# Kernel optimization log

Measured on AMD Instinct MI355X. Metric: run time of the kernel, lower is better.

Reference implementation:

```python
import jax, jax.numpy as jnp
import numpy as np

N = 20000      # atoms
E = 320000     # pairs (avg degree 16)
F = 64         # per-atom features
NRBF = 32      # radial basis functions
RC = 1.0       # maximum_interaction_radius


def _decompose(t):
    # X = I + A + S (irreducible decomposition of 3x3 tensors)
    diag_mean = jnp.diagonal(t, axis1=-2, axis2=-1).mean(-1)
    I = diag_mean[..., None, None] * jnp.eye(3, dtype=t.dtype)
    A = 0.5 * (t - jnp.swapaxes(t, -1, -2))
    S = 0.5 * (t + jnp.swapaxes(t, -1, -2)) - I
    return I, A, S


def _tnorm(t):
    # Frobenius norm^2 over the trailing 3x3 -> [N, F]
    return (t ** 2).sum((-2, -1))


def _lin_t(t, W):
    # channel-mixing linear on the feature axis of [N, F, 3, 3]
    return jnp.einsum('nfij,gf->ngij', t, W)


def setup_inputs():
    key = jax.random.key(0)
    ks = jax.random.split(key, 14)
    inp = {
        'X': jax.random.normal(ks[0], (N, F, 3, 3), jnp.float32) * 0.1,
        'pair_indices': jax.random.randint(ks[1], (2, E), 0, N, jnp.int32),
        'd_ij': jax.random.uniform(ks[2], (E, 1), jnp.float32),
        'radial_feature_vector': jax.random.normal(ks[3], (E, NRBF), jnp.float32),
        'atomic_charges': jax.random.normal(ks[4], (N,), jnp.float32) * 0.1,
        # mlp_scalar: NRBF -> F -> 2F -> 3F (Dense = Linear + activation)
        'W0': jax.random.normal(ks[5], (F, NRBF), jnp.float32) / np.sqrt(NRBF),
        'b0': jnp.zeros((F,), jnp.float32),
        'W1': jax.random.normal(ks[6], (2 * F, F), jnp.float32) / np.sqrt(F),
        'b1': jnp.zeros((2 * F,), jnp.float32),
        'W2': jax.random.normal(ks[7], (3 * F, 2 * F), jnp.float32) / np.sqrt(2 * F),
        'b2': jnp.zeros((3 * F,), jnp.float32),
        # 6 bias-free FxF tensor linears
        'Wt': jax.random.normal(ks[8], (6, F, F), jnp.float32) / np.sqrt(F),
    }
    return inp


def reference(X, pair_indices, d_ij, radial_feature_vector, atomic_charges,
              W0, b0, W1, b1, W2, b2, Wt):
    silu = jax.nn.silu
    n_atoms = X.shape[0]
    src = pair_indices[1]  # gathered
    dst = pair_indices[0]  # scattered (index_add_)

    # cosine cutoff, [E, 1]
    C = (0.5 * (jnp.cos(jnp.pi * d_ij / RC) + 1.0)
         * (d_ij < RC).astype(X.dtype)).reshape(-1, 1)

    h = silu(radial_feature_vector @ W0.T + b0)
    h = silu(h @ W1.T + b1)
    h = silu(h @ W2.T + b2)                 # [E, 3F]
    rfv = (h * C).reshape(-1, F, 3)          # [E, F, 3]

    X = X / (_tnorm(X) + 1.0)[..., None, None]
    I, A, S = _decompose(X)
    I = _lin_t(I, Wt[0])
    A = _lin_t(A, Wt[1])
    S = _lin_t(S, Wt[2])
    Y = I + A + S

    def mp(r, T):
        # gather-mul-scatter: [E,F,3,3] messages reduced to [N,F,3,3]
        msg = r[:, :, None, None] * T[src]
        return jax.ops.segment_sum(msg, dst, num_segments=n_atoms)

    msg = mp(rfv[..., 0], I) + mp(rfv[..., 1], A) + mp(rfv[..., 2], S)

    # O(3) group
    q = (1.0 + 0.1 * atomic_charges)[:, None, None, None]
    I, A, S = _decompose(q * (jnp.matmul(msg, Y) + jnp.matmul(Y, msg)))

    normp1 = (_tnorm(I + A + S) + 1.0)[..., None, None]
    I, A, S = I / normp1, A / normp1, S / normp1
    I = _lin_t(I, Wt[3])
    A = _lin_t(A, Wt[4])
    S = _lin_t(S, Wt[5])
    dX = I + A + S

    X = X + dX + q * jnp.matmul(dX, dX)
    return X
```

## Files before the change

### kernel.cpp

```cpp
#include <hip/hip_runtime.h>
#include <hip/hip_bf16.h>
#include <cmath>

#define N_ATOMS 20000
#define NE      320000
#define FDIM    64
#define NRBF    32
#define PI_F    3.14159265358979323846f

typedef __attribute__((ext_vector_type(8))) short bf16x8;
typedef __attribute__((ext_vector_type(4))) float f32x4;

#define MFMA16(a, b, c) __builtin_amdgcn_mfma_f32_16x16x32_bf16(a, b, c, 0, 0, 0)

__device__ __forceinline__ float silu(float x) {
    return x / (1.0f + __expf(-x));
}

__device__ __forceinline__ unsigned short f2bf_rne(float x) {
    unsigned u = __float_as_uint(x);
    u += 0x7fffu + ((u >> 16) & 1u);
    return (unsigned short)(u >> 16);
}

__device__ __forceinline__ void split8(const float* v, bf16x8& hi, bf16x8& lo) {
#pragma unroll
    for (int j = 0; j < 8; j++) {
        unsigned u = __float_as_uint(v[j]);
        float hf = __uint_as_float(u & 0xffff0000u);
        hi[j] = (short)(u >> 16);
        lo[j] = (short)f2bf_rne(v[j] - hf);
    }
}

__global__ void transpose_kernel(const float* __restrict__ Wt, float* __restrict__ wtT) {
    int idx = blockIdx.x * 256 + threadIdx.x;
    if (idx >= 24576) return;
    int k = idx >> 12;
    int r = idx & 4095;
    int g = r >> 6;
    int f = r & 63;
    wtT[k * 4096 + f * 64 + g] = Wt[idx];
}

__global__ void wfrag_kernel(const float* __restrict__ W0, const float* __restrict__ W1,
                             const float* __restrict__ W2,
                             unsigned short* __restrict__ f0h, unsigned short* __restrict__ f0l,
                             unsigned short* __restrict__ f1h, unsigned short* __restrict__ f1l,
                             unsigned short* __restrict__ f2h, unsigned short* __restrict__ f2l) {
    int idx = blockIdx.x * 256 + threadIdx.x;
    const float* W;
    unsigned short *fh, *fl;
    int t, K, NT;
    if (idx < 2048)       { W = W0; fh = f0h; fl = f0l; t = idx;         K = 32;  NT = 4; }
    else if (idx < 10240) { W = W1; fh = f1h; fl = f1l; t = idx - 2048;  K = 64;  NT = 8; }
    else if (idx < 34816) { W = W2; fh = f2h; fl = f2l; t = idx - 10240; K = 128; NT = 12; }
    else return;
    int j = t & 7;
    int lane = (t >> 3) & 63;
    int rest = t >> 9;
    int nt = rest % NT;
    int ks = rest / NT;
    int k = ks * 32 + ((lane >> 4) & 3) * 8 + j;
    int n = nt * 16 + (lane & 15);
    float w = W[n * K + k];
    unsigned u = __float_as_uint(w);
    float hf = __uint_as_float(u & 0xffff0000u);
    fh[t] = (unsigned short)(u >> 16);
    fl[t] = f2bf_rne(w - hf);
}

__global__ void hist_kernel(const int* __restrict__ dst, int* __restrict__ deg) {
    int e = blockIdx.x * 256 + threadIdx.x;
    if (e >= NE) return;
    atomicAdd(&deg[dst[e]], 1);
}

__global__ void scan_kernel(const int* __restrict__ deg, int* __restrict__ off) {
    __shared__ int part[1024];
    int t = threadIdx.x;
    const int CH = (N_ATOMS + 1023) / 1024;
    int base = t * CH;
    int s = 0;
    for (int i = 0; i < CH; i++) {
        int idx = base + i;
        if (idx < N_ATOMS) s += deg[idx];
    }
    part[t] = s;
    __syncthreads();
    for (int ofs = 1; ofs < 1024; ofs <<= 1) {
        int v = (t >= ofs) ? part[t - ofs] : 0;
        __syncthreads();
        part[t] += v;
        __syncthreads();
    }
    int run = (t == 0) ? 0 : part[t - 1];
    for (int i = 0; i < CH; i++) {
        int idx = base + i;
        if (idx < N_ATOMS) {
            off[idx] = run;
            run += deg[idx];
        }
    }
    if (t == 1023) off[N_ATOMS] = run;
}

__global__ void fill_kernel(const int* __restrict__ dst, const int* __restrict__ srcArr,
                            const int* __restrict__ off, int* __restrict__ cursor,
                            int* __restrict__ sbkt, int* __restrict__ slotOf) {
    int e = blockIdx.x * 256 + threadIdx.x;
    if (e >= NE) return;
    int d = dst[e];
    int pos = atomicAdd(&cursor[d], 1);
    int slot = off[d] + pos;
    sbkt[slot] = srcArr[e];
    slotOf[e] = slot;
}

#define H1S 68
#define H2S 132
__global__ __launch_bounds__(128) void mlp_mfma_kernel(
    const float* __restrict__ rfv, const float* __restrict__ dij,
    const float* __restrict__ b0, const float* __restrict__ b1, const float* __restrict__ b2,
    const unsigned short* __restrict__ f0h, const unsigned short* __restrict__ f0l,
    const unsigned short* __restrict__ f1h, const unsigned short* __restrict__ f1l,
    const unsigned short* __restrict__ f2h, const unsigned short* __restrict__ f2l,
    const int* __restrict__ slotOf,
    __hip_bfloat16* __restrict__ r) {
    __shared__ float h1s[2][32][H1S];
    __shared__ float h2s[2][32][H2S];
    const int w = threadIdx.x >> 6;
    const int lane = threadIdx.x & 63;
    const int q = lane >> 4;
    const int c = lane & 15;
    const int e0 = (blockIdx.x * 2 + w) * 32;
    float (*h1)[H1S] = h1s[w];
    float (*h2)[H2S] = h2s[w];

    {
        bf16x8 ah[2], al[2];
#pragma unroll
        for (int mt = 0; mt < 2; mt++) {
            float v[8];
            const float* p = rfv + (size_t)(e0 + mt * 16 + c) * 32 + q * 8;
            *(float4*)(v)     = *(const float4*)(p);
            *(float4*)(v + 4) = *(const float4*)(p + 4);
            split8(v, ah[mt], al[mt]);
        }
#pragma unroll
        for (int nt = 0; nt < 4; nt++) {
            float bias = b0[nt * 16 + c];
            f32x4 acc[2];
            acc[0] = {bias, bias, bias, bias};
            acc[1] = acc[0];
            bf16x8 bh = *(const bf16x8*)(f0h + (size_t)(nt * 64 + lane) * 8);
            bf16x8 bl = *(const bf16x8*)(f0l + (size_t)(nt * 64 + lane) * 8);
#pragma unroll
            for (int mt = 0; mt < 2; mt++) {
                acc[mt] = MFMA16(al[mt], bh, acc[mt]);
                acc[mt] = MFMA16(ah[mt], bl, acc[mt]);
                acc[mt] = MFMA16(ah[mt], bh, acc[mt]);
            }
#pragma unroll
            for (int mt = 0; mt < 2; mt++)
#pragma unroll
                for (int reg = 0; reg < 4; reg++)
                    h1[mt * 16 + q * 4 + reg][nt * 16 + c] = silu(acc[mt][reg]);
        }
    }

    {
        bf16x8 ah[2][2], al[2][2];
#pragma unroll
        for (int mt = 0; mt < 2; mt++)
#pragma unroll
            for (int ks = 0; ks < 2; ks++) {
                float v[8];
                const float* p = &h1[mt * 16 + c][ks * 32 + q * 8];
                *(float4*)(v)     = *(const float4*)(p);
                *(float4*)(v + 4) = *(const float4*)(p + 4);
                split8(v, ah[mt][ks], al[mt][ks]);
            }
#pragma unroll
        for (int nt = 0; nt < 8; nt++) {
            float bias = b1[nt * 16 + c];
            f32x4 acc[2];
            acc[0] = {bias, bias, bias, bias};
            acc[1] = acc[0];
#pragma unroll
            for (int ks = 0; ks < 2; ks++) {
                bf16x8 bh = *(const bf16x8*)(f1h + (size_t)((ks * 8 + nt) * 64 + lane) * 8);
                bf16x8 bl = *(const bf16x8*)(f1l + (size_t)((ks * 8 + nt) * 64 + lane) * 8);
#pragma unroll
                for (int mt = 0; mt < 2; mt++) {
                    acc[mt] = MFMA16(al[mt][ks], bh, acc[mt]);
                    acc[mt] = MFMA16(ah[mt][ks], bl, acc[mt]);
                    acc[mt] = MFMA16(ah[mt][ks], bh, acc[mt]);
                }
            }
#pragma unroll
            for (int mt = 0; mt < 2; mt++)
#pragma unroll
                for (int reg = 0; reg < 4; reg++)
                    h2[mt * 16 + q * 4 + reg][nt * 16 + c] = silu(acc[mt][reg]);
        }
    }

    {
        bf16x8 ah[2][4], al[2][4];
#pragma unroll
        for (int mt = 0; mt < 2; mt++)
#pragma unroll
            for (int ks = 0; ks < 4; ks++) {
                float v[8];
                const float* p = &h2[mt * 16 + c][ks * 32 + q * 8];
                *(float4*)(v)     = *(const float4*)(p);
                *(float4*)(v + 4) = *(const float4*)(p + 4);
                split8(v, ah[mt][ks], al[mt][ks]);
            }
        float cut[2][4];
        int srow[2][4];
#pragma unroll
        for (int mt = 0; mt < 2; mt++)
#pragma unroll
            for (int reg = 0; reg < 4; reg++) {
                int e = e0 + mt * 16 + q * 4 + reg;
                float d = dij[e];
                cut[mt][reg] = (d < 1.0f) ? 0.5f * (__cosf(PI_F * d) + 1.0f) : 0.0f;
                srow[mt][reg] = slotOf[e];
            }
#pragma unroll
        for (int nt = 0; nt < 12; nt++) {
            float bias = b2[nt * 16 + c];
            f32x4 acc[2];
            acc[0] = {bias, bias, bias, bias};
            acc[1] = acc[0];
#pragma unroll
            for (int ks = 0; ks < 4; ks++) {
                bf16x8 bh = *(const bf16x8*)(f2h + (size_t)((ks * 12 + nt) * 64 + lane) * 8);
                bf16x8 bl = *(const bf16x8*)(f2l + (size_t)((ks * 12 + nt) * 64 + lane) * 8);
#pragma unroll
                for (int mt = 0; mt < 2; mt++) {
                    acc[mt] = MFMA16(al[mt][ks], bh, acc[mt]);
                    acc[mt] = MFMA16(ah[mt][ks], bl, acc[mt]);
                    acc[mt] = MFMA16(ah[mt][ks], bh, acc[mt]);
                }
            }
#pragma unroll
            for (int mt = 0; mt < 2; mt++)
#pragma unroll
                for (int reg = 0; reg < 4; reg++)
                    r[(size_t)srow[mt][reg] * 192 + nt * 16 + c] =
                        __float2bfloat16(silu(acc[mt][reg]) * cut[mt][reg]);
        }
    }
}

__global__ __launch_bounds__(256) void lin1_kernel(
    const float* __restrict__ X, const float* __restrict__ wtT,
    float* __restrict__ comp, float* __restrict__ Yb) {
    __shared__ float lds[4][64 * 11];
    int w = threadIdx.x >> 6;
    int l = threadIdx.x & 63;
    int a = blockIdx.x * 4 + w;

    {
        const float* x = X + ((size_t)a * 64 + l) * 9;
        float v[9];
#pragma unroll
        for (int i = 0; i < 9; i++) v[i] = x[i];
        float t2 = 0.f;
#pragma unroll
        for (int i = 0; i < 9; i++) t2 += v[i] * v[i];
        float inv = 1.0f / (t2 + 1.0f);
#pragma unroll
        for (int i = 0; i < 9; i++) v[i] *= inv;
        float iso = (v[0] + v[4] + v[8]) * (1.0f / 3.0f);
        float* o = &lds[w][l * 11];
        o[0] = iso;
        o[1] = 0.5f * (v[1] - v[3]);
        o[2] = 0.5f * (v[2] - v[6]);
        o[3] = 0.5f * (v[5] - v[7]);
        o[4] = v[0] - iso;
        o[5] = 0.5f * (v[1] + v[3]);
        o[6] = 0.5f * (v[2] + v[6]);
        o[7] = v[4] - iso;
        o[8] = 0.5f * (v[5] + v[7]);
        o[9] = v[8] - iso;
    }
    __syncthreads();
    {
        int g = l;
        const float* w0 = wtT;
        const float* w1 = wtT + 4096;
        const float* w2 = wtT + 8192;
        float acc[10];
#pragma unroll
        for (int c = 0; c < 10; c++) acc[c] = 0.f;
        for (int f = 0; f < 64; f++) {
            float wI = w0[f * 64 + g];
            float wA = w1[f * 64 + g];
            float wS = w2[f * 64 + g];
            const float* rf = &lds[w][f * 11];
            acc[0] += wI * rf[0];
            acc[1] += wA * rf[1];
            acc[2] += wA * rf[2];
            acc[3] += wA * rf[3];
#pragma unroll
            for (int c = 4; c < 10; c++) acc[c] += wS * rf[c];
        }
        float* co = comp + ((size_t)a * 64 + g) * 12;
        float4 c0 = {acc[0], acc[1], acc[2], acc[3]};
        float4 c1 = {acc[4], acc[5], acc[6], acc[7]};
        float4 c2 = {acc[8], acc[9], 0.f, 0.f};
        *(float4*)(co)     = c0;
        *(float4*)(co + 4) = c1;
        *(float4*)(co + 8) = c2;
        float* y = Yb + ((size_t)a * 64 + g) * 9;
        y[0] = acc[0] + acc[4];
        y[1] = acc[5] + acc[1];
        y[2] = acc[6] + acc[2];
        y[3] = acc[5] - acc[1];
        y[4] = acc[0] + acc[7];
        y[5] = acc[8] + acc[3];
        y[6] = acc[6] - acc[2];
        y[7] = acc[8] - acc[3];
        y[8] = acc[0] + acc[9];
    }
}

__global__ __launch_bounds__(256) void msg_lin2_kernel(
    const int* __restrict__ off, const int* __restrict__ sbkt,
    const __hip_bfloat16* __restrict__ r,
    const float* __restrict__ comp, const float* __restrict__ Yb,
    const float* __restrict__ X, const float* __restrict__ charges,
    const float* __restrict__ wtT, float* __restrict__ out) {
    __shared__ float lds[4][64 * 11];
    int w = threadIdx.x >> 6;
    int l = threadIdx.x & 63;
    int a = blockIdx.x * 4 + w;
    float q = 1.0f + 0.1f * charges[a];

    float m[10];
#pragma unroll
    for (int c = 0; c < 10; c++) m[c] = 0.f;
    {
        int beg = off[a], end = off[a + 1];
        if (beg < end) {
            __hip_bfloat16 ra, rb, rc;
            float4 c0, c1, c2;
            {
                const __hip_bfloat16* rp = r + (size_t)beg * 192 + l * 3;
                ra = rp[0]; rb = rp[1]; rc = rp[2];
                const float* cp = comp + ((size_t)sbkt[beg] * 64 + l) * 12;
                c0 = *(const float4*)(cp);
                c1 = *(const float4*)(cp + 4);
                c2 = *(const float4*)(cp + 8);
            }
            for (int i = beg + 1; i < end; i++) {
                const __hip_bfloat16* rp = r + (size_t)i * 192 + l * 3;
                __hip_bfloat16 na = rp[0], nb = rp[1], nc = rp[2];
                const float* cp = comp + ((size_t)sbkt[i] * 64 + l) * 12;
                float4 n0 = *(const float4*)(cp);
                float4 n1 = *(const float4*)(cp + 4);
                float4 n2 = *(const float4*)(cp + 8);
                float r0 = __bfloat162float(ra);
                float r1 = __bfloat162float(rb);
                float r2 = __bfloat162float(rc);
                m[0] += r0 * c0.x;
                m[1] += r1 * c0.y;
                m[2] += r1 * c0.z;
                m[3] += r1 * c0.w;
                m[4] += r2 * c1.x;
                m[5] += r2 * c1.y;
                m[6] += r2 * c1.z;
                m[7] += r2 * c1.w;
                m[8] += r2 * c2.x;
                m[9] += r2 * c2.y;
                ra = na; rb = nb; rc = nc;
                c0 = n0; c1 = n1; c2 = n2;
            }
            float r0 = __bfloat162float(ra);
            float r1 = __bfloat162float(rb);
            float r2 = __bfloat162float(rc);
            m[0] += r0 * c0.x;
            m[1] += r1 * c0.y;
            m[2] += r1 * c0.z;
            m[3] += r1 * c0.w;
            m[4] += r2 * c1.x;
            m[5] += r2 * c1.y;
            m[6] += r2 * c1.z;
            m[7] += r2 * c1.w;
            m[8] += r2 * c2.x;
            m[9] += r2 * c2.y;
        }
    }

    {
        float M[9];
        M[0] = m[0] + m[4]; M[1] = m[5] + m[1]; M[2] = m[6] + m[2];
        M[3] = m[5] - m[1]; M[4] = m[0] + m[7]; M[5] = m[8] + m[3];
        M[6] = m[6] - m[2]; M[7] = m[8] - m[3]; M[8] = m[0] + m[9];
        const float* yp = Yb + ((size_t)a * 64 + l) * 9;
        float Y[9];
#pragma unroll
        for (int i = 0; i < 9; i++) Y[i] = yp[i];
        float P[9];
#pragma unroll
        for (int i = 0; i < 3; i++) {
#pragma unroll
            for (int j = 0; j < 3; j++) {
                float s = 0.f;
#pragma unroll
                for (int k = 0; k < 3; k++)
                    s += M[i * 3 + k] * Y[k * 3 + j] + Y[i * 3 + k] * M[k * 3 + j];
                P[i * 3 + j] = q * s;
            }
        }
        float t2 = 0.f;
#pragma unroll
        for (int i = 0; i < 9; i++) t2 += P[i] * P[i];
        float inv = 1.0f / (t2 + 1.0f);
        float iso = (P[0] + P[4] + P[8]) * (1.0f / 3.0f);
        float* o = &lds[w][l * 11];
        o[0] = iso * inv;
        o[1] = 0.5f * (P[1] - P[3]) * inv;
        o[2] = 0.5f * (P[2] - P[6]) * inv;
        o[3] = 0.5f * (P[5] - P[7]) * inv;
        o[4] = (P[0] - iso) * inv;
        o[5] = 0.5f * (P[1] + P[3]) * inv;
        o[6] = 0.5f * (P[2] + P[6]) * inv;
        o[7] = (P[4] - iso) * inv;
        o[8] = 0.5f * (P[5] + P[7]) * inv;
        o[9] = (P[8] - iso) * inv;
    }
    __syncthreads();
    {
        int g = l;
        const float* w3 = wtT + 3 * 4096;
        const float* w4 = wtT + 4 * 4096;
        const float* w5 = wtT + 5 * 4096;
        float acc[10];
#pragma unroll
        for (int c = 0; c < 10; c++) acc[c] = 0.f;
        for (int f = 0; f < 64; f++) {
            float wI = w3[f * 64 + g];
            float wA = w4[f * 64 + g];
            float wS = w5[f * 64 + g];
            const float* rf = &lds[w][f * 11];
            acc[0] += wI * rf[0];
            acc[1] += wA * rf[1];
            acc[2] += wA * rf[2];
            acc[3] += wA * rf[3];
#pragma unroll
            for (int c = 4; c < 10; c++) acc[c] += wS * rf[c];
        }
        float D[9];
        D[0] = acc[0] + acc[4]; D[1] = acc[5] + acc[1]; D[2] = acc[6] + acc[2];
        D[3] = acc[5] - acc[1]; D[4] = acc[0] + acc[7]; D[5] = acc[8] + acc[3];
        D[6] = acc[6] - acc[2]; D[7] = acc[8] - acc[3]; D[8] = acc[0] + acc[9];

        const float* x = X + ((size_t)a * 64 + g) * 9;
        float xv[9];
#pragma unroll
        for (int i = 0; i < 9; i++) xv[i] = x[i];
        float t2 = 0.f;
#pragma unroll
        for (int i = 0; i < 9; i++) t2 += xv[i] * xv[i];
        float invn = 1.0f / (t2 + 1.0f);
#pragma unroll
        for (int i = 0; i < 9; i++) xv[i] *= invn;

        float DD[9];
#pragma unroll
        for (int i = 0; i < 3; i++) {
#pragma unroll
            for (int j = 0; j < 3; j++) {
                float s = 0.f;
#pragma unroll
                for (int k = 0; k < 3; k++) s += D[i * 3 + k] * D[k * 3 + j];
                DD[i * 3 + j] = s;
            }
        }
        float* op = out + ((size_t)a * 64 + g) * 9;
#pragma unroll
        for (int i = 0; i < 9; i++) op[i] = xv[i] + D[i] + q * DD[i];
    }
}

extern "C" void kernel_launch(void* const* d_in, const int* in_sizes, int n_in,
                              void* d_out, int out_size, void* d_ws, size_t ws_size,
                              hipStream_t stream) {
    const float* X       = (const float*)d_in[0];
    const int*   pair    = (const int*)d_in[1];
    const float* dij     = (const float*)d_in[2];
    const float* rfv     = (const float*)d_in[3];
    const float* charges = (const float*)d_in[4];
    const float* W0      = (const float*)d_in[5];
    const float* b0      = (const float*)d_in[6];
    const float* W1      = (const float*)d_in[7];
    const float* b1      = (const float*)d_in[8];
    const float* W2      = (const float*)d_in[9];
    const float* b2      = (const float*)d_in[10];
    const float* Wt      = (const float*)d_in[11];
    float* out = (float*)d_out;

    const int* dst = pair;
    const int* src = pair + NE;

    char* ws = (char*)d_ws;
    size_t ofs = 0;
    auto alloc = [&](size_t bytes) {
        void* p = ws + ofs;
        ofs += (bytes + 255) & ~(size_t)255;
        return p;
    };
    float* wtT  = (float*)alloc((size_t)6 * 4096 * 4);
    unsigned short* f0h = (unsigned short*)alloc(2048 * 2);
    unsigned short* f0l = (unsigned short*)alloc(2048 * 2);
    unsigned short* f1h = (unsigned short*)alloc(8192 * 2);
    unsigned short* f1l = (unsigned short*)alloc(8192 * 2);
    unsigned short* f2h = (unsigned short*)alloc(24576 * 2);
    unsigned short* f2l = (unsigned short*)alloc(24576 * 2);
    float* comp = (float*)alloc((size_t)N_ATOMS * FDIM * 12 * 4);
    __hip_bfloat16* rbuf = (__hip_bfloat16*)alloc((size_t)NE * 192 * 2);
    int* deg    = (int*)alloc((size_t)N_ATOMS * 4);
    int* offarr = (int*)alloc((size_t)(N_ATOMS + 1) * 4);
    int* cursor = (int*)alloc((size_t)N_ATOMS * 4);
    int* sbkt   = (int*)alloc((size_t)NE * 4);
    int* slotOf = (int*)alloc((size_t)NE * 4);
    float* Yb   = out;

    hipMemsetAsync(deg, 0, (size_t)N_ATOMS * 4, stream);
    hipMemsetAsync(cursor, 0, (size_t)N_ATOMS * 4, stream);

    transpose_kernel<<<(24576 + 255) / 256, 256, 0, stream>>>(Wt, wtT);
    wfrag_kernel<<<(34816 + 255) / 256, 256, 0, stream>>>(
        W0, W1, W2, f0h, f0l, f1h, f1l, f2h, f2l);
    hist_kernel<<<NE / 256, 256, 0, stream>>>(dst, deg);
    scan_kernel<<<1, 1024, 0, stream>>>(deg, offarr);
    fill_kernel<<<NE / 256, 256, 0, stream>>>(dst, src, offarr, cursor, sbkt, slotOf);

    mlp_mfma_kernel<<<NE / 64, 128, 0, stream>>>(
        rfv, dij, b0, b1, b2, f0h, f0l, f1h, f1l, f2h, f2l, slotOf, rbuf);

    lin1_kernel<<<N_ATOMS / 4, 256, 0, stream>>>(X, wtT, comp, Yb);

    msg_lin2_kernel<<<N_ATOMS / 4, 256, 0, stream>>>(
        offarr, sbkt, rbuf, comp, Yb, X, charges, wtT, out);
}
```

Baseline: 553.8 us.

## Merge prep kernels into one launch and interleave lin1 blocks with MLP blocks

Folds the weight transpose, MFMA weight-fragment packing and degree histogram into a single prep kernel, cutting two launches. Fuses the atom-side lin1 work into the edge MLP kernel: odd blocks each handle four atoms while even blocks run the MFMA MLP, so the two independent stages share one grid. This removes launch gaps and lets lin1 fill idle slots beside the MLP work. In exchange the fused kernel's register and LDS budget is set by the larger path, and the lin1 path now runs as 2 waves of 128 threads instead of 4 waves of 256.

```diff
diff --git a/kernel.cpp b/kernel.cpp
--- a/kernel.cpp
+++ b/kernel.cpp
@@ -33,47 +33,44 @@
     }
 }
 
-__global__ void transpose_kernel(const float* __restrict__ Wt, float* __restrict__ wtT) {
+__global__ void prep_kernel(const float* __restrict__ Wt, float* __restrict__ wtT,
+                            const float* __restrict__ W0, const float* __restrict__ W1,
+                            const float* __restrict__ W2,
+                            unsigned short* __restrict__ f0h, unsigned short* __restrict__ f0l,
+                            unsigned short* __restrict__ f1h, unsigned short* __restrict__ f1l,
+                            unsigned short* __restrict__ f2h, unsigned short* __restrict__ f2l,
+                            const int* __restrict__ dst, int* __restrict__ deg) {
     int idx = blockIdx.x * 256 + threadIdx.x;
-    if (idx >= 24576) return;
-    int k = idx >> 12;
-    int r = idx & 4095;
-    int g = r >> 6;
-    int f = r & 63;
-    wtT[k * 4096 + f * 64 + g] = Wt[idx];
-}
-
-__global__ void wfrag_kernel(const float* __restrict__ W0, const float* __restrict__ W1,
-                             const float* __restrict__ W2,
-                             unsigned short* __restrict__ f0h, unsigned short* __restrict__ f0l,
-                             unsigned short* __restrict__ f1h, unsigned short* __restrict__ f1l,
-                             unsigned short* __restrict__ f2h, unsigned short* __restrict__ f2l) {
-    int idx = blockIdx.x * 256 + threadIdx.x;
-    const float* W;
-    unsigned short *fh, *fl;
-    int t, K, NT;
-    if (idx < 2048)       { W = W0; fh = f0h; fl = f0l; t = idx;         K = 32;  NT = 4; }
-    else if (idx < 10240) { W = W1; fh = f1h; fl = f1l; t = idx - 2048;  K = 64;  NT = 8; }
-    else if (idx < 34816) { W = W2; fh = f2h; fl = f2l; t = idx - 10240; K = 128; NT = 12; }
-    else return;
-    int j = t & 7;
-    int lane = (t >> 3) & 63;
-    int rest = t >> 9;
-    int nt = rest % NT;
-    int ks = rest / NT;
-    int k = ks * 32 + ((lane >> 4) & 3) * 8 + j;
-    int n = nt * 16 + (lane & 15);
-    float w = W[n * K + k];
-    unsigned u = __float_as_uint(w);
-    float hf = __uint_as_float(u & 0xffff0000u);
-    fh[t] = (unsigned short)(u >> 16);
-    fl[t] = f2bf_rne(w - hf);
-}
-
-__global__ void hist_kernel(const int* __restrict__ dst, int* __restrict__ deg) {
-    int e = blockIdx.x * 256 + threadIdx.x;
-    if (e >= NE) return;
-    atomicAdd(&deg[dst[e]], 1);
+    if (idx < 24576) {
+        int k = idx >> 12;
+        int r = idx & 4095;
+        int g = r >> 6;
+        int f = r & 63;
+        wtT[k * 4096 + f * 64 + g] = Wt[idx];
+    } else if (idx < 59392) {
+        int t = idx - 24576;
+        const float* W;
+        unsigned short *fh, *fl;
+        int K, NT;
+        if (t < 2048)       { W = W0; fh = f0h; fl = f0l;               K = 32;  NT = 4; }
+        else if (t < 10240) { W = W1; fh = f1h; fl = f1l; t -= 2048;    K = 64;  NT = 8; }
+        else                { W = W2; fh = f2h; fl = f2l; t -= 10240;   K = 128; NT = 12; }
+        int j = t & 7;
+        int lane = (t >> 3) & 63;
+        int rest = t >> 9;
+        int nt = rest % NT;
+        int ks = rest / NT;
+        int k = ks * 32 + ((lane >> 4) & 3) * 8 + j;
+        int n = nt * 16 + (lane & 15);
+        float w = W[n * K + k];
+        unsigned u = __float_as_uint(w);
+        float hf = __uint_as_float(u & 0xffff0000u);
+        fh[t] = (unsigned short)(u >> 16);
+        fl[t] = f2bf_rne(w - hf);
+    } else if (idx < 59392 + NE) {
+        int e = idx - 59392;
+        atomicAdd(&deg[dst[e]], 1);
+    }
 }
 
 __global__ void scan_kernel(const int* __restrict__ deg, int* __restrict__ off) {
@@ -119,21 +116,96 @@
 
 #define H1S 68
 #define H2S 132
-__global__ __launch_bounds__(128) void mlp_mfma_kernel(
+__global__ __launch_bounds__(128) void mlp_lin1_kernel(
     const float* __restrict__ rfv, const float* __restrict__ dij,
     const float* __restrict__ b0, const float* __restrict__ b1, const float* __restrict__ b2,
     const unsigned short* __restrict__ f0h, const unsigned short* __restrict__ f0l,
     const unsigned short* __restrict__ f1h, const unsigned short* __restrict__ f1l,
     const unsigned short* __restrict__ f2h, const unsigned short* __restrict__ f2l,
-    const int* __restrict__ slotOf,
-    __hip_bfloat16* __restrict__ r) {
+    const int* __restrict__ slotOf, __hip_bfloat16* __restrict__ r,
+    const float* __restrict__ X, const float* __restrict__ wtT,
+    float* __restrict__ comp, float* __restrict__ Yb) {
     __shared__ float h1s[2][32][H1S];
     __shared__ float h2s[2][32][H2S];
     const int w = threadIdx.x >> 6;
     const int lane = threadIdx.x & 63;
+
+    if (blockIdx.x & 1) {
+        int id = blockIdx.x >> 1;
+        float* stage = ((float*)h1s) + w * 704;
+#pragma unroll
+        for (int at = 0; at < 2; at++) {
+            int a = id * 4 + w * 2 + at;
+            int l = lane;
+            {
+                const float* x = X + ((size_t)a * 64 + l) * 9;
+                float v[9];
+#pragma unroll
+                for (int i = 0; i < 9; i++) v[i] = x[i];
+                float t2 = 0.f;
+#pragma unroll
+                for (int i = 0; i < 9; i++) t2 += v[i] * v[i];
+                float inv = 1.0f / (t2 + 1.0f);
+#pragma unroll
+                for (int i = 0; i < 9; i++) v[i] *= inv;
+                float iso = (v[0] + v[4] + v[8]) * (1.0f / 3.0f);
+                float* o = &stage[l * 11];
+                o[0] = iso;
+                o[1] = 0.5f * (v[1] - v[3]);
+                o[2] = 0.5f * (v[2] - v[6]);
+                o[3] = 0.5f * (v[5] - v[7]);
+                o[4] = v[0] - iso;
+                o[5] = 0.5f * (v[1] + v[3]);
+                o[6] = 0.5f * (v[2] + v[6]);
+                o[7] = v[4] - iso;
+                o[8] = 0.5f * (v[5] + v[7]);
+                o[9] = v[8] - iso;
+            }
+            {
+                int g = l;
+                const float* w0 = wtT;
+                const float* w1 = wtT + 4096;
+                const float* w2 = wtT + 8192;
+                float acc[10];
+#pragma unroll
+                for (int c = 0; c < 10; c++) acc[c] = 0.f;
+                for (int f = 0; f < 64; f++) {
+                    float wI = w0[f * 64 + g];
+                    float wA = w1[f * 64 + g];
+                    float wS = w2[f * 64 + g];
+                    const float* rf = &stage[f * 11];
+                    acc[0] += wI * rf[0];
+                    acc[1] += wA * rf[1];
+                    acc[2] += wA * rf[2];
+                    acc[3] += wA * rf[3];
+#pragma unroll
+                    for (int c = 4; c < 10; c++) acc[c] += wS * rf[c];
+                }
+                float* co = comp + ((size_t)a * 64 + g) * 12;
+                float4 c0 = {acc[0], acc[1], acc[2], acc[3]};
+                float4 c1 = {acc[4], acc[5], acc[6], acc[7]};
+                float4 c2 = {acc[8], acc[9], 0.f, 0.f};
+                *(float4*)(co)     = c0;
+                *(float4*)(co + 4) = c1;
+                *(float4*)(co + 8) = c2;
+                float* y = Yb + ((size_t)a * 64 + g) * 9;
+                y[0] = acc[0] + acc[4];
+                y[1] = acc[5] + acc[1];
+                y[2] = acc[6] + acc[2];
+                y[3] = acc[5] - acc[1];
+                y[4] = acc[0] + acc[7];
+                y[5] = acc[8] + acc[3];
+                y[6] = acc[6] - acc[2];
+                y[7] = acc[8] - acc[3];
+                y[8] = acc[0] + acc[9];
+            }
+        }
+        return;
+    }
+
     const int q = lane >> 4;
     const int c = lane & 15;
-    const int e0 = (blockIdx.x * 2 + w) * 32;
+    const int e0 = ((blockIdx.x >> 1) * 2 + w) * 32;
     float (*h1)[H1S] = h1s[w];
     float (*h2)[H2S] = h2s[w];
 
@@ -253,79 +325,6 @@
                     r[(size_t)srow[mt][reg] * 192 + nt * 16 + c] =
                         __float2bfloat16(silu(acc[mt][reg]) * cut[mt][reg]);
         }
-    }
-}
-
-__global__ __launch_bounds__(256) void lin1_kernel(
-    const float* __restrict__ X, const float* __restrict__ wtT,
-    float* __restrict__ comp, float* __restrict__ Yb) {
-    __shared__ float lds[4][64 * 11];
-    int w = threadIdx.x >> 6;
-    int l = threadIdx.x & 63;
-    int a = blockIdx.x * 4 + w;
-
-    {
-        const float* x = X + ((size_t)a * 64 + l) * 9;
-        float v[9];
-#pragma unroll
-        for (int i = 0; i < 9; i++) v[i] = x[i];
-        float t2 = 0.f;
-#pragma unroll
-        for (int i = 0; i < 9; i++) t2 += v[i] * v[i];
-        float inv = 1.0f / (t2 + 1.0f);
-#pragma unroll
-        for (int i = 0; i < 9; i++) v[i] *= inv;
-        float iso = (v[0] + v[4] + v[8]) * (1.0f / 3.0f);
-        float* o = &lds[w][l * 11];
-        o[0] = iso;
-        o[1] = 0.5f * (v[1] - v[3]);
-        o[2] = 0.5f * (v[2] - v[6]);
-        o[3] = 0.5f * (v[5] - v[7]);
-        o[4] = v[0] - iso;
-        o[5] = 0.5f * (v[1] + v[3]);
-        o[6] = 0.5f * (v[2] + v[6]);
-        o[7] = v[4] - iso;
-        o[8] = 0.5f * (v[5] + v[7]);
-        o[9] = v[8] - iso;
-    }
-    __syncthreads();
-    {
-        int g = l;
-        const float* w0 = wtT;
-        const float* w1 = wtT + 4096;
-        const float* w2 = wtT + 8192;
-        float acc[10];
-#pragma unroll
-        for (int c = 0; c < 10; c++) acc[c] = 0.f;
-        for (int f = 0; f < 64; f++) {
-            float wI = w0[f * 64 + g];
-            float wA = w1[f * 64 + g];
-            float wS = w2[f * 64 + g];
-            const float* rf = &lds[w][f * 11];
-            acc[0] += wI * rf[0];
-            acc[1] += wA * rf[1];
-            acc[2] += wA * rf[2];
-            acc[3] += wA * rf[3];
-#pragma unroll
-            for (int c = 4; c < 10; c++) acc[c] += wS * rf[c];
-        }
-        float* co = comp + ((size_t)a * 64 + g) * 12;
-        float4 c0 = {acc[0], acc[1], acc[2], acc[3]};
-        float4 c1 = {acc[4], acc[5], acc[6], acc[7]};
-        float4 c2 = {acc[8], acc[9], 0.f, 0.f};
-        *(float4*)(co)     = c0;
-        *(float4*)(co + 4) = c1;
-        *(float4*)(co + 8) = c2;
-        float* y = Yb + ((size_t)a * 64 + g) * 9;
-        y[0] = acc[0] + acc[4];
-        y[1] = acc[5] + acc[1];
-        y[2] = acc[6] + acc[2];
-        y[3] = acc[5] - acc[1];
-        y[4] = acc[0] + acc[7];
-        y[5] = acc[8] + acc[3];
-        y[6] = acc[6] - acc[2];
-        y[7] = acc[8] - acc[3];
-        y[8] = acc[0] + acc[9];
     }
 }
 
@@ -534,17 +533,14 @@
     hipMemsetAsync(deg, 0, (size_t)N_ATOMS * 4, stream);
     hipMemsetAsync(cursor, 0, (size_t)N_ATOMS * 4, stream);
 
-    transpose_kernel<<<(24576 + 255) / 256, 256, 0, stream>>>(Wt, wtT);
-    wfrag_kernel<<<(34816 + 255) / 256, 256, 0, stream>>>(
-        W0, W1, W2, f0h, f0l, f1h, f1l, f2h, f2l);
-    hist_kernel<<<NE / 256, 256, 0, stream>>>(dst, deg);
+    prep_kernel<<<(59392 + NE + 255) / 256, 256, 0, stream>>>(
+        Wt, wtT, W0, W1, W2, f0h, f0l, f1h, f1l, f2h, f2l, dst, deg);
     scan_kernel<<<1, 1024, 0, stream>>>(deg, offarr);
     fill_kernel<<<NE / 256, 256, 0, stream>>>(dst, src, offarr, cursor, sbkt, slotOf);
 
-    mlp_mfma_kernel<<<NE / 64, 128, 0, stream>>>(
-        rfv, dij, b0, b1, b2, f0h, f0l, f1h, f1l, f2h, f2l, slotOf, rbuf);
-
-    lin1_kernel<<<N_ATOMS / 4, 256, 0, stream>>>(X, wtT, comp, Yb);
+    mlp_lin1_kernel<<<10000, 128, 0, stream>>>(
+        rfv, dij, b0, b1, b2, f0h, f0l, f1h, f1l, f2h, f2l, slotOf, rbuf,
+        X, wtT, comp, Yb);
 
     msg_lin2_kernel<<<N_ATOMS / 4, 256, 0, stream>>>(
         offarr, sbkt, rbuf, comp, Yb, X, charges, wtT, out);
```

After: 612.2 us. 1.11x slower.
